# Optimization experiments

Hardware: AMD Instinct MI355X
Metric: run time of the kernel (lower is better)

The kernel has to match this reference:

```python
import jax, jax.numpy as jnp
import numpy as np

HEAD_NUM = 16
HEAD_SIZE = 64
D_MODEL = 1024
B, N = 8, 1024
MASK_PENALTY = 1e8


def setup_inputs() -> dict:
    key = jax.random.key(0)
    k1, k2, k3 = jax.random.split(key, 3)
    inputs = jax.random.normal(k1, (B, N, D_MODEL), dtype=jnp.float32)
    mask = jax.random.randint(k2, (B, N), 0, 2).astype(jnp.float32)
    # glorot-uniform-ish init for kernel [H, 3, d_model, head_size]
    limit = float(np.sqrt(6.0 / (D_MODEL + HEAD_SIZE)))
    kernel = jax.random.uniform(k3, (HEAD_NUM, 3, D_MODEL, HEAD_SIZE),
                                dtype=jnp.float32, minval=-limit, maxval=limit)
    return {"inputs": inputs, "mask": mask, "kernel": kernel}


def reference(inputs, mask, kernel):
    # inputs: [B,N,d], kernel: [H,3,d,s]
    q = jnp.einsum('bnd,hds->bhns', inputs, kernel[:, 0])
    k = jnp.einsum('bnd,hds->bhns', inputs, kernel[:, 1])
    v = jnp.einsum('bnd,hds->bhns', inputs, kernel[:, 2])
    # NOTE: original never applies 1/sqrt(head_size) scaling (faithful).
    scores = jnp.einsum('bhns,bhms->bhnm', q, k)  # [B,H,N,N]
    # additive mask: outer product of padding mask, penalty on masked pairs
    pair_mask = mask[:, None, :, None] * mask[:, None, None, :]  # [B,1,N,N]
    scores = scores - MASK_PENALTY * (1.0 - pair_mask)
    attn = jax.nn.softmax(scores, axis=-1)
    out = jnp.einsum('bhnm,bhms->bhns', attn, v)  # [B,H,N,s]
    # original permutes to [B,N,s,H] then flattens -> head axis fastest
    out = jnp.transpose(out, (0, 2, 3, 1))  # [B,N,s,H]
    return out.reshape(out.shape[0], out.shape[1], HEAD_SIZE * HEAD_NUM)
```

## Files before the change

kernel.cpp:

```cpp
#include <hip/hip_runtime.h>
#include <math.h>

#define BB 8
#define NN 1024
#define DD 1024
#define HH 16
#define SS 64
#define BH (BB*HH)

typedef _Float16 half8 __attribute__((ext_vector_type(8)));
typedef _Float16 half4v __attribute__((ext_vector_type(4)));
typedef float floatx4 __attribute__((ext_vector_type(4)));

#define MFMA16(A, B, C) __builtin_amdgcn_mfma_f32_16x16x32_f16((A), (B), (C), 0, 0, 0)

__device__ __forceinline__ void gload16(const _Float16* g, _Float16* l) {
    __builtin_amdgcn_global_load_lds(
        (const __attribute__((address_space(1))) void*)g,
        (__attribute__((address_space(3))) void*)l,
        16, 0, 0);
}

__global__ __launch_bounds__(256) void split_x(
    const float* __restrict__ X, _Float16* __restrict__ Xh, _Float16* __restrict__ Xl)
{
    int idx = (blockIdx.x * 256 + threadIdx.x) * 4;
    float4 x4 = *(const float4*)(X + idx);
    float xs[4] = {x4.x, x4.y, x4.z, x4.w};
    half4v h, l;
    #pragma unroll
    for (int i = 0; i < 4; i++) {
        _Float16 hi = (_Float16)xs[i];
        h[i] = hi;
        l[i] = (_Float16)(xs[i] - (float)hi);
    }
    *(half4v*)(Xh + idx) = h;
    *(half4v*)(Xl + idx) = l;
}

__global__ __launch_bounds__(256) void split_wt(
    const float* __restrict__ W, _Float16* __restrict__ Wth, _Float16* __restrict__ Wtl)
{
    __shared__ float tile[64][68];
    const int hc = blockIdx.x, d0 = blockIdx.y * 64;
    const int t = threadIdx.x;
    {
        int i = t >> 2, sq = (t & 3) * 16;
        const float* src = W + ((size_t)hc * DD + d0 + i) * SS + sq;
        #pragma unroll
        for (int u = 0; u < 4; u++) {
            float4 v = *(const float4*)(src + 4 * u);
            tile[i][sq + 4 * u + 0] = v.x; tile[i][sq + 4 * u + 1] = v.y;
            tile[i][sq + 4 * u + 2] = v.z; tile[i][sq + 4 * u + 3] = v.w;
        }
    }
    __syncthreads();
    {
        int s = t >> 2, jq = (t & 3) * 16;
        _Float16 hbuf[16], lbuf[16];
        #pragma unroll
        for (int u = 0; u < 16; u++) {
            float x = tile[jq + u][s];
            _Float16 hi = (_Float16)x;
            hbuf[u] = hi;
            lbuf[u] = (_Float16)(x - (float)hi);
        }
        size_t off = (size_t)hc * SS * DD + (size_t)s * DD + d0 + jq;
        *(half8*)(Wth + off)     = *(half8*)(hbuf);
        *(half8*)(Wth + off + 8) = *(half8*)(hbuf + 8);
        *(half8*)(Wtl + off)     = *(half8*)(lbuf);
        *(half8*)(Wtl + off + 8) = *(half8*)(lbuf + 8);
    }
}

__global__ __launch_bounds__(256, 2) void qkv_mfma(
    const _Float16* __restrict__ Xh, const _Float16* __restrict__ Xl,
    const _Float16* __restrict__ Wth, const _Float16* __restrict__ Wtl,
    _Float16* __restrict__ Qh, _Float16* __restrict__ Ql,
    _Float16* __restrict__ Kh, _Float16* __restrict__ Kl,
    _Float16* __restrict__ Vt)
{
    const int flat = blockIdx.y * 64 + blockIdx.x;
    const int swz  = (flat & 7) * 192 + (flat >> 3);
    const int bx = swz & 63;
    const int by = swz >> 6;
    const int hc0 = by * 2;
    const int r0  = bx * 128;

    const int tid = threadIdx.x;
    const int wave = tid >> 6, lane = tid & 63;
    const int l16 = lane & 15, quad = lane >> 4;
    const int wr = wave >> 1, wc = wave & 1;

    __shared__ _Float16 sAh[128 * 32];
    __shared__ _Float16 sAl[128 * 32];
    __shared__ _Float16 sBh[128 * 32];
    __shared__ _Float16 sBl[128 * 32];

    floatx4 acc[4][4];
    #pragma unroll
    for (int i = 0; i < 4; i++)
        #pragma unroll
        for (int j = 0; j < 4; j++) acc[i][j] = (floatx4){0.f, 0.f, 0.f, 0.f};

    const _Float16* Ab_h = Xh  + (size_t)r0 * DD;
    const _Float16* Ab_l = Xl  + (size_t)r0 * DD;
    const _Float16* Bb_h = Wth + (size_t)hc0 * SS * DD;
    const _Float16* Bb_l = Wtl + (size_t)hc0 * SS * DD;

    for (int k0 = 0; k0 < DD; k0 += 32) {
        #pragma unroll
        for (int i = 0; i < 2; i++) {
            const int g = tid + 256 * i;
            const int row = g >> 2, kc = (g & 3) * 8;
            const size_t go = (size_t)row * DD + k0 + kc;
            gload16(Ab_h + go, &sAh[g * 8]);
            gload16(Ab_l + go, &sAl[g * 8]);
            gload16(Bb_h + go, &sBh[g * 8]);
            gload16(Bb_l + go, &sBl[g * 8]);
        }
        __syncthreads();

        half8 Ah[4], Al[4], Bh[4], Bl[4];
        #pragma unroll
        for (int t = 0; t < 4; t++) {
            const int ar = wr * 64 + 16 * t + l16;
            const int br = wc * 64 + 16 * t + l16;
            Ah[t] = *(const half8*)&sAh[ar * 32 + quad * 8];
            Al[t] = *(const half8*)&sAl[ar * 32 + quad * 8];
            Bh[t] = *(const half8*)&sBh[br * 32 + quad * 8];
            Bl[t] = *(const half8*)&sBl[br * 32 + quad * 8];
        }
        #pragma unroll
        for (int i = 0; i < 4; i++)
            #pragma unroll
            for (int j = 0; j < 4; j++)
                acc[i][j] = MFMA16(Ah[i], Bh[j], acc[i][j]);
        #pragma unroll
        for (int i = 0; i < 4; i++)
            #pragma unroll
            for (int j = 0; j < 4; j++)
                acc[i][j] = MFMA16(Ah[i], Bl[j], acc[i][j]);
        #pragma unroll
        for (int i = 0; i < 4; i++)
            #pragma unroll
            for (int j = 0; j < 4; j++)
                acc[i][j] = MFMA16(Al[i], Bh[j], acc[i][j]);
        __syncthreads();
    }

    const int hc = hc0 + wc;
    const int h = hc / 3, c = hc % 3;
    const int rowbase = r0 + wr * 64;
    if (c == 2) {
        #pragma unroll
        for (int i = 0; i < 4; i++)
            #pragma unroll
            for (int j = 0; j < 4; j++) {
                int tok0 = rowbase + 16 * i + 4 * quad;
                int b = tok0 >> 10, n0 = tok0 & 1023;
                half4v pk;
                #pragma unroll
                for (int r = 0; r < 4; r++) pk[r] = (_Float16)acc[i][j][r];
                *(half4v*)(Vt + ((size_t)(b * HH + h) * SS + 16 * j + l16) * NN + n0) = pk;
            }
    } else {
        _Float16* Ph = (c == 0) ? Qh : Kh;
        _Float16* Pl = (c == 0) ? Ql : Kl;
        #pragma unroll
        for (int i = 0; i < 4; i++)
            #pragma unroll
            for (int j = 0; j < 4; j++)
                #pragma unroll
                for (int r = 0; r < 4; r++) {
                    int tok = rowbase + 16 * i + 4 * quad + r;
                    int b = tok >> 10, n = tok & 1023;
                    float v = acc[i][j][r];
                    _Float16 vh = (_Float16)v;
                    _Float16 vl = (_Float16)(v - (float)vh);
                    size_t off = ((size_t)(b * HH + h) * NN + n) * SS + 16 * j + l16;
                    Ph[off] = vh; Pl[off] = vl;
                }
    }
}

__global__ __launch_bounds__(256) void attn_mfma(
    const _Float16* __restrict__ Qh, const _Float16* __restrict__ Ql,
    const _Float16* __restrict__ Kh, const _Float16* __restrict__ Kl,
    const _Float16* __restrict__ Vt,
    const float* __restrict__ mask,
    float* __restrict__ out)
{
    const int bh = blockIdx.x, qt = blockIdx.y;
    const int b = bh >> 4, h = bh & 15;
    const int tid = threadIdx.x;
    const int wave = tid >> 6, lane = tid & 63;
    const int l16 = lane & 15, quad = lane >> 4;

    __shared__ float Ms[NN];
    __shared__ _Float16 KhS[64 * 64];
    __shared__ _Float16 KlS[64 * 64];
    __shared__ _Float16 VS [64 * 64];
    __shared__ _Float16 Plds[4][32][72];

    *(float4*)&Ms[tid * 4] = *(const float4*)(mask + b * NN + tid * 4);

    half8 G[6];
    auto stage_load = [&](int kt_) {
        #pragma unroll
        for (int i = 0; i < 2; i++) {
            int g = tid + 256 * i;
            int row = g >> 3;
            int c = (g & 7) ^ (row & 7);
            size_t ko = ((size_t)bh * NN + kt_ * 64 + row) * SS + c * 8;
            G[i]     = *(const half8*)(Kh + ko);
            G[2 + i] = *(const half8*)(Kl + ko);
            G[4 + i] = *(const half8*)(Vt + ((size_t)bh * SS + row) * NN
                                       + (size_t)kt_ * 64 + c * 8);
        }
    };
    auto stage_store = [&]() {
        #pragma unroll
        for (int i = 0; i < 2; i++) {
            int g = tid + 256 * i;
            *(half8*)&KhS[g * 8] = G[i];
            *(half8*)&KlS[g * 8] = G[2 + i];
            *(half8*)&VS [g * 8] = G[4 + i];
        }
    };

    stage_load(0);
    stage_store();
    __syncthreads();

    const int qrow0 = qt * 128 + wave * 32;
    half8 Aqh[2][2], Aql[2][2];
    #pragma unroll
    for (int g = 0; g < 2; g++) {
        const size_t qbase = ((size_t)bh * NN + qrow0 + 16 * g + l16) * SS + quad * 8;
        Aqh[g][0] = *(const half8*)(Qh + qbase);
        Aqh[g][1] = *(const half8*)(Qh + qbase + 32);
        Aql[g][0] = *(const half8*)(Ql + qbase);
        Aql[g][1] = *(const half8*)(Ql + qbase + 32);
    }

    float qm[2], m_old[2], l_sum[2];
    floatx4 accO[2][4];
    #pragma unroll
    for (int g = 0; g < 2; g++) {
        qm[g] = Ms[qrow0 + 16 * g + l16];
        m_old[g] = -3.0e38f;
        l_sum[g] = 0.f;
        #pragma unroll
        for (int j = 0; j < 4; j++) accO[g][j] = (floatx4){0.f, 0.f, 0.f, 0.f};
    }

    const int sw = l16 & 7;

    for (int kt = 0; kt < 16; kt++) {
        if (kt < 15) stage_load(kt + 1);

        floatx4 accS[2][4];
        #pragma unroll
        for (int g = 0; g < 2; g++)
            #pragma unroll
            for (int jt = 0; jt < 4; jt++) accS[g][jt] = (floatx4){0.f, 0.f, 0.f, 0.f};
        #pragma unroll
        for (int jt = 0; jt < 4; jt++) {
            const int rowK = jt * 16 + l16;
            const _Float16* krh = &KhS[rowK * 64];
            const _Float16* krl = &KlS[rowK * 64];
            half8 Bh0 = *(const half8*)&krh[((quad    ) ^ sw) * 8];
            half8 Bh1 = *(const half8*)&krh[((quad + 4) ^ sw) * 8];
            half8 Bl0 = *(const half8*)&krl[((quad    ) ^ sw) * 8];
            half8 Bl1 = *(const half8*)&krl[((quad + 4) ^ sw) * 8];
            #pragma unroll
            for (int g = 0; g < 2; g++) {
                accS[g][jt] = MFMA16(Bh0, Aqh[g][0], accS[g][jt]);
                accS[g][jt] = MFMA16(Bh1, Aqh[g][1], accS[g][jt]);
                accS[g][jt] = MFMA16(Bl0, Aqh[g][0], accS[g][jt]);
                accS[g][jt] = MFMA16(Bl1, Aqh[g][1], accS[g][jt]);
                accS[g][jt] = MFMA16(Bh0, Aql[g][0], accS[g][jt]);
                accS[g][jt] = MFMA16(Bh1, Aql[g][1], accS[g][jt]);
            }
        }

        float km[4][4];
        #pragma unroll
        for (int jt = 0; jt < 4; jt++) {
            float4 k4 = *(const float4*)&Ms[kt * 64 + jt * 16 + quad * 4];
            km[jt][0] = k4.x; km[jt][1] = k4.y; km[jt][2] = k4.z; km[jt][3] = k4.w;
        }
        #pragma unroll
        for (int g = 0; g < 2; g++)
            #pragma unroll
            for (int jt = 0; jt < 4; jt++)
                #pragma unroll
                for (int r = 0; r < 4; r++)
                    accS[g][jt][r] -= 1.0e8f * (1.0f - qm[g] * km[jt][r]);

        #pragma unroll
        for (int g = 0; g < 2; g++) {
            float a0 = fmaxf(fmaxf(accS[g][0][0], accS[g][0][1]),
                             fmaxf(accS[g][0][2], accS[g][0][3]));
            float a1 = fmaxf(fmaxf(accS[g][1][0], accS[g][1][1]),
                             fmaxf(accS[g][1][2], accS[g][1][3]));
            float a2 = fmaxf(fmaxf(accS[g][2][0], accS[g][2][1]),
                             fmaxf(accS[g][2][2], accS[g][2][3]));
            float a3 = fmaxf(fmaxf(accS[g][3][0], accS[g][3][1]),
                             fmaxf(accS[g][3][2], accS[g][3][3]));
            float mt = fmaxf(fmaxf(a0, a1), fmaxf(a2, a3));
            mt = fmaxf(mt, __shfl_xor(mt, 16, 64));
            mt = fmaxf(mt, __shfl_xor(mt, 32, 64));
            float mn = fmaxf(m_old[g], mt);

            float sj[4];
            #pragma unroll
            for (int jt = 0; jt < 4; jt++) {
                float p0 = __expf(accS[g][jt][0] - mn);
                float p1 = __expf(accS[g][jt][1] - mn);
                float p2 = __expf(accS[g][jt][2] - mn);
                float p3 = __expf(accS[g][jt][3] - mn);
                accS[g][jt][0] = p0; accS[g][jt][1] = p1;
                accS[g][jt][2] = p2; accS[g][jt][3] = p3;
                sj[jt] = (p0 + p1) + (p2 + p3);
            }
            float ls = (sj[0] + sj[1]) + (sj[2] + sj[3]);
            ls += __shfl_xor(ls, 16, 64);
            ls += __shfl_xor(ls, 32, 64);

            if (__any(mt > m_old[g])) {
                float alpha = __expf(m_old[g] - mn);
                m_old[g] = mn;
                l_sum[g] = l_sum[g] * alpha + ls;
                float alphaO[4];
                #pragma unroll
                for (int r = 0; r < 4; r++)
                    alphaO[r] = __shfl(alpha, quad * 4 + r, 64);
                #pragma unroll
                for (int j = 0; j < 4; j++)
                    #pragma unroll
                    for (int r = 0; r < 4; r++)
                        accO[g][j][r] *= alphaO[r];
            } else {
                l_sum[g] = l_sum[g] + ls;
            }

            #pragma unroll
            for (int jt = 0; jt < 4; jt++) {
                half4v pk;
                #pragma unroll
                for (int r = 0; r < 4; r++) pk[r] = (_Float16)accS[g][jt][r];
                *(half4v*)&Plds[wave][16 * g + l16][jt * 16 + quad * 4] = pk;
            }
        }

        #pragma unroll
        for (int ks = 0; ks < 2; ks++) {
            half8 Ap[2];
            #pragma unroll
            for (int g = 0; g < 2; g++)
                Ap[g] = *(const half8*)&Plds[wave][16 * g + l16][ks * 32 + quad * 8];
            #pragma unroll
            for (int j = 0; j < 4; j++) {
                half8 Bv = *(const half8*)&VS[(j * 16 + l16) * 64
                                              + (((ks * 4 + quad) ^ sw) * 8)];
                #pragma unroll
                for (int g = 0; g < 2; g++)
                    accO[g][j] = MFMA16(Ap[g], Bv, accO[g][j]);
            }
        }

        if (kt < 15) {
            __syncthreads();
            stage_store();
            __syncthreads();
        }
    }

    #pragma unroll
    for (int g = 0; g < 2; g++) {
        float inv[4];
        #pragma unroll
        for (int r = 0; r < 4; r++)
            inv[r] = 1.f / __shfl(l_sum[g], quad * 4 + r, 64);
        #pragma unroll
        for (int r = 0; r < 4; r++) {
            int qrow = qrow0 + 16 * g + quad * 4 + r;
            #pragma unroll
            for (int j = 0; j < 4; j++)
                out[((size_t)(b * NN + qrow)) * (SS * HH) + (j * 16 + l16) * HH + h] =
                    accO[g][j][r] * inv[r];
        }
    }
}

__global__ __launch_bounds__(256) void qkv_kernel(
    const float* __restrict__ X, const float* __restrict__ W, float* __restrict__ qkv)
{
    const int ttile = blockIdx.x;
    const int hc    = blockIdx.y;
    const int h     = hc / 3, c = hc % 3;
    const int tid = threadIdx.x;
    const int tx = tid & 15, ty = tid >> 4;
    __shared__ float As[32][68];
    __shared__ float Bs[32][68];
    const float* Wb = W + (size_t)hc * DD * SS;
    const int row0 = ttile * 64;
    float acc[4][4];
    #pragma unroll
    for (int i = 0; i < 4; i++)
        #pragma unroll
        for (int j = 0; j < 4; j++) acc[i][j] = 0.f;
    for (int k0 = 0; k0 < DD; k0 += 32) {
        #pragma unroll
        for (int l = 0; l < 2; l++) {
            int i = tid + l * 256;
            int r = i >> 3;
            int kq = (i & 7) * 4;
            float4 x4 = *(const float4*)(X + (size_t)(row0 + r) * DD + k0 + kq);
            As[kq + 0][r] = x4.x; As[kq + 1][r] = x4.y;
            As[kq + 2][r] = x4.z; As[kq + 3][r] = x4.w;
        }
        #pragma unroll
        for (int l = 0; l < 2; l++) {
            int i = tid + l * 256;
            int kr = i >> 4;
            int sq = (i & 15) * 4;
            *(float4*)&Bs[kr][sq] = *(const float4*)(Wb + (size_t)(k0 + kr) * SS + sq);
        }
        __syncthreads();
        #pragma unroll
        for (int kk = 0; kk < 32; kk++) {
            float4 a4 = *(const float4*)&As[kk][ty * 4];
            float4 b4 = *(const float4*)&Bs[kk][tx * 4];
            float a[4] = {a4.x, a4.y, a4.z, a4.w};
            float bb[4] = {b4.x, b4.y, b4.z, b4.w};
            #pragma unroll
            for (int i = 0; i < 4; i++)
                #pragma unroll
                for (int j = 0; j < 4; j++)
                    acc[i][j] = fmaf(a[i], bb[j], acc[i][j]);
        }
        __syncthreads();
    }
    float* outp = qkv + (size_t)c * BH * NN * SS;
    #pragma unroll
    for (int i = 0; i < 4; i++) {
        int tg = row0 + ty * 4 + i;
        int b = tg >> 10, n = tg & 1023;
        float4 v4 = make_float4(acc[i][0], acc[i][1], acc[i][2], acc[i][3]);
        *(float4*)(outp + ((size_t)(b * HH + h) * NN + n) * SS + tx * 4) = v4;
    }
}

__global__ __launch_bounds__(256) void attn_kernel(
    const float* __restrict__ qkv,
    const float* __restrict__ mask,
    float* __restrict__ out)
{
    const int qt = blockIdx.x, h = blockIdx.y, b = blockIdx.z;
    const int tid = threadIdx.x;
    const int tx = tid & 15, ty = tid >> 4;
    const int bh = b * HH + h;
    const float* Q = qkv + (size_t)bh * NN * SS;
    const float* K = qkv + (size_t)BH * NN * SS + (size_t)bh * NN * SS;
    const float* V = qkv + 2 * (size_t)BH * NN * SS + (size_t)bh * NN * SS;

    __shared__ float QsT[64][68];
    __shared__ float KsT[64][68];
    __shared__ float Vs [64][68];
    __shared__ float PsT[64][68];
    __shared__ float Ms[NN];

    {
        float4 mm = *(const float4*)(mask + b * NN + tid * 4);
        *(float4*)&Ms[tid * 4] = mm;
    }
    #pragma unroll
    for (int l = 0; l < 4; l++) {
        int i = tid + l * 256;
        int r = i >> 4, sq = (i & 15) * 4;
        float4 x4 = *(const float4*)(Q + (size_t)(qt * 64 + r) * SS + sq);
        QsT[sq + 0][r] = x4.x; QsT[sq + 1][r] = x4.y;
        QsT[sq + 2][r] = x4.z; QsT[sq + 3][r] = x4.w;
    }
    __syncthreads();

    float m_old[4], l_sum[4], O[4][4], qm[4];
    #pragma unroll
    for (int i = 0; i < 4; i++) {
        qm[i] = Ms[qt * 64 + ty * 4 + i];
        m_old[i] = -3.0e38f; l_sum[i] = 0.f;
        #pragma unroll
        for (int j = 0; j < 4; j++) O[i][j] = 0.f;
    }

    for (int kt = 0; kt < 16; kt++) {
        #pragma unroll
        for (int l = 0; l < 4; l++) {
            int i = tid + l * 256;
            int r = i >> 4, sq = (i & 15) * 4;
            float4 k4 = *(const float4*)(K + (size_t)(kt * 64 + r) * SS + sq);
            KsT[sq + 0][r] = k4.x; KsT[sq + 1][r] = k4.y;
            KsT[sq + 2][r] = k4.z; KsT[sq + 3][r] = k4.w;
            float4 v4 = *(const float4*)(V + (size_t)(kt * 64 + r) * SS + sq);
            *(float4*)&Vs[r][sq] = v4;
        }
        __syncthreads();

        float sc[4][4];
        #pragma unroll
        for (int i = 0; i < 4; i++)
            #pragma unroll
            for (int j = 0; j < 4; j++) sc[i][j] = 0.f;
        #pragma unroll 8
        for (int s = 0; s < 64; s++) {
            float4 a4 = *(const float4*)&QsT[s][ty * 4];
            float4 b4 = *(const float4*)&KsT[s][tx * 4];
            float a[4] = {a4.x, a4.y, a4.z, a4.w};
            float bb[4] = {b4.x, b4.y, b4.z, b4.w};
            #pragma unroll
            for (int i = 0; i < 4; i++)
                #pragma unroll
                for (int j = 0; j < 4; j++)
                    sc[i][j] = fmaf(a[i], bb[j], sc[i][j]);
        }
        float km[4];
        #pragma unroll
        for (int j = 0; j < 4; j++) km[j] = Ms[kt * 64 + tx * 4 + j];
        #pragma unroll
        for (int i = 0; i < 4; i++)
            #pragma unroll
            for (int j = 0; j < 4; j++) {
                float pen = 1.0e8f * (1.0f - qm[i] * km[j]);
                sc[i][j] = sc[i][j] - pen;
            }

        #pragma unroll
        for (int i = 0; i < 4; i++) {
            float mt = fmaxf(fmaxf(sc[i][0], sc[i][1]), fmaxf(sc[i][2], sc[i][3]));
            #pragma unroll
            for (int off = 1; off < 16; off <<= 1)
                mt = fmaxf(mt, __shfl_xor(mt, off, 64));
            float mn = fmaxf(m_old[i], mt);
            float alpha = __expf(m_old[i] - mn);
            float p[4];
            #pragma unroll
            for (int j = 0; j < 4; j++) p[j] = __expf(sc[i][j] - mn);
            float ls = (p[0] + p[1]) + (p[2] + p[3]);
            #pragma unroll
            for (int off = 1; off < 16; off <<= 1)
                ls += __shfl_xor(ls, off, 64);
            l_sum[i] = l_sum[i] * alpha + ls;
            m_old[i] = mn;
            #pragma unroll
            for (int j = 0; j < 4; j++) {
                O[i][j] *= alpha;
                PsT[tx * 4 + j][ty * 4 + i] = p[j];
            }
        }
        __syncthreads();

        #pragma unroll 8
        for (int kj = 0; kj < 64; kj++) {
            float4 p4 = *(const float4*)&PsT[kj][ty * 4];
            float4 v4 = *(const float4*)&Vs[kj][tx * 4];
            float p[4] = {p4.x, p4.y, p4.z, p4.w};
            float vv[4] = {v4.x, v4.y, v4.z, v4.w};
            #pragma unroll
            for (int i = 0; i < 4; i++)
                #pragma unroll
                for (int j = 0; j < 4; j++)
                    O[i][j] = fmaf(p[i], vv[j], O[i][j]);
        }
        __syncthreads();
    }

    #pragma unroll
    for (int i = 0; i < 4; i++) {
        int qrow = qt * 64 + ty * 4 + i;
        float inv = 1.f / l_sum[i];
        #pragma unroll
        for (int j = 0; j < 4; j++) {
            int s = tx * 4 + j;
            out[((size_t)(b * NN + qrow)) * (SS * HH) + s * HH + h] = O[i][j] * inv;
        }
    }
}

extern "C" void kernel_launch(void* const* d_in, const int* in_sizes, int n_in,
                              void* d_out, int out_size, void* d_ws, size_t ws_size,
                              hipStream_t stream) {
    const float* X    = (const float*)d_in[0];
    const float* mask = (const float*)d_in[1];
    const float* W    = (const float*)d_in[2];
    float* out = (float*)d_out;

    const size_t x_elems  = (size_t)BB * NN * DD;
    const size_t w_elems  = (size_t)HH * 3 * SS * DD;
    const size_t qk_elems = (size_t)BH * NN * SS;
    const size_t need_fast = (2 * x_elems + 2 * w_elems + 5 * qk_elems) * sizeof(_Float16);

    if (ws_size >= need_fast) {
        _Float16* Xh  = (_Float16*)d_ws;
        _Float16* Xl  = Xh  + x_elems;
        _Float16* Wth = Xl  + x_elems;
        _Float16* Wtl = Wth + w_elems;
        _Float16* Qh  = Wtl + w_elems;
        _Float16* Ql  = Qh  + qk_elems;
        _Float16* Kh  = Ql  + qk_elems;
        _Float16* Kl  = Kh  + qk_elems;
        _Float16* Vt  = Kl  + qk_elems;

        split_x<<<dim3((unsigned)(x_elems / 1024)), dim3(256), 0, stream>>>(X, Xh, Xl);
        split_wt<<<dim3(48, 16), dim3(256), 0, stream>>>(W, Wth, Wtl);
        qkv_mfma<<<dim3(64, 24), dim3(256), 0, stream>>>(Xh, Xl, Wth, Wtl, Qh, Ql, Kh, Kl, Vt);
        attn_mfma<<<dim3(128, 8), dim3(256), 0, stream>>>(Qh, Ql, Kh, Kl, Vt, mask, out);
    } else if (ws_size >= 3ull * BH * NN * SS * sizeof(float)) {
        float* qkv = (float*)d_ws;
        qkv_kernel<<<dim3(128, 48), dim3(256), 0, stream>>>(X, W, qkv);
        attn_kernel<<<dim3(16, 16, 8), dim3(256), 0, stream>>>(qkv, mask, out);
    }
}
```

Measured before the change: 414.8 us.

## Read K and V tiles directly from global memory instead of LDS staging

Removes the shared-memory staging of K (high/low halves) and transposed V tiles, along with the two block-wide barriers per key tile. Each wave now loads its MFMA B operands straight from global memory, relying on L1/L2 caching for reuse across the four waves. This cuts LDS traffic, barrier stalls and LDS footprint, which may raise occupancy, but it quadruples global and cache load requests and drops the register-prefetch overlap that hid load latency.

```diff
diff --git a/kernel.cpp b/kernel.cpp
--- a/kernel.cpp
+++ b/kernel.cpp
@@ -198,40 +198,14 @@
     const int l16 = lane & 15, quad = lane >> 4;
 
     __shared__ float Ms[NN];
-    __shared__ _Float16 KhS[64 * 64];
-    __shared__ _Float16 KlS[64 * 64];
-    __shared__ _Float16 VS [64 * 64];
     __shared__ _Float16 Plds[4][32][72];
 
     *(float4*)&Ms[tid * 4] = *(const float4*)(mask + b * NN + tid * 4);
-
-    half8 G[6];
-    auto stage_load = [&](int kt_) {
-        #pragma unroll
-        for (int i = 0; i < 2; i++) {
-            int g = tid + 256 * i;
-            int row = g >> 3;
-            int c = (g & 7) ^ (row & 7);
-            size_t ko = ((size_t)bh * NN + kt_ * 64 + row) * SS + c * 8;
-            G[i]     = *(const half8*)(Kh + ko);
-            G[2 + i] = *(const half8*)(Kl + ko);
-            G[4 + i] = *(const half8*)(Vt + ((size_t)bh * SS + row) * NN
-                                       + (size_t)kt_ * 64 + c * 8);
-        }
-    };
-    auto stage_store = [&]() {
-        #pragma unroll
-        for (int i = 0; i < 2; i++) {
-            int g = tid + 256 * i;
-            *(half8*)&KhS[g * 8] = G[i];
-            *(half8*)&KlS[g * 8] = G[2 + i];
-            *(half8*)&VS [g * 8] = G[4 + i];
-        }
-    };
-
-    stage_load(0);
-    stage_store();
     __syncthreads();
+
+    const _Float16* Kbh = Kh + (size_t)bh * NN * SS;
+    const _Float16* Kbl = Kl + (size_t)bh * NN * SS;
+    const _Float16* Vb  = Vt + (size_t)bh * SS * NN;
 
     const int qrow0 = qt * 128 + wave * 32;
     half8 Aqh[2][2], Aql[2][2];
@@ -255,11 +229,7 @@
         for (int j = 0; j < 4; j++) accO[g][j] = (floatx4){0.f, 0.f, 0.f, 0.f};
     }
 
-    const int sw = l16 & 7;
-
     for (int kt = 0; kt < 16; kt++) {
-        if (kt < 15) stage_load(kt + 1);
-
         floatx4 accS[2][4];
         #pragma unroll
         for (int g = 0; g < 2; g++)
@@ -267,13 +237,11 @@
             for (int jt = 0; jt < 4; jt++) accS[g][jt] = (floatx4){0.f, 0.f, 0.f, 0.f};
         #pragma unroll
         for (int jt = 0; jt < 4; jt++) {
-            const int rowK = jt * 16 + l16;
-            const _Float16* krh = &KhS[rowK * 64];
-            const _Float16* krl = &KlS[rowK * 64];
-            half8 Bh0 = *(const half8*)&krh[((quad    ) ^ sw) * 8];
-            half8 Bh1 = *(const half8*)&krh[((quad + 4) ^ sw) * 8];
-            half8 Bl0 = *(const half8*)&krl[((quad    ) ^ sw) * 8];
-            half8 Bl1 = *(const half8*)&krl[((quad + 4) ^ sw) * 8];
+            const size_t krow = (size_t)(kt * 64 + jt * 16 + l16) * SS + quad * 8;
+            half8 Bh0 = *(const half8*)(Kbh + krow);
+            half8 Bh1 = *(const half8*)(Kbh + krow + 32);
+            half8 Bl0 = *(const half8*)(Kbl + krow);
+            half8 Bl1 = *(const half8*)(Kbl + krow + 32);
             #pragma unroll
             for (int g = 0; g < 2; g++) {
                 accS[g][jt] = MFMA16(Bh0, Aqh[g][0], accS[g][jt]);
@@ -363,18 +331,12 @@
                 Ap[g] = *(const half8*)&Plds[wave][16 * g + l16][ks * 32 + quad * 8];
             #pragma unroll
             for (int j = 0; j < 4; j++) {
-                half8 Bv = *(const half8*)&VS[(j * 16 + l16) * 64
-                                              + (((ks * 4 + quad) ^ sw) * 8)];
+                half8 Bv = *(const half8*)(Vb + (size_t)(j * 16 + l16) * NN
+                                           + kt * 64 + (ks * 4 + quad) * 8);
                 #pragma unroll
                 for (int g = 0; g < 2; g++)
                     accO[g][j] = MFMA16(Ap[g], Bv, accO[g][j]);
             }
-        }
-
-        if (kt < 15) {
-            __syncthreads();
-            stage_store();
-            __syncthreads();
         }
     }
 
```

Result: slower. 519.0 us (+25.1%).
